# Kernel tuning notes

Measured on AMD Instinct MI355X. Metric: run time of the kernel, lower is better.

Reference implementation:

```python
import jax, jax.numpy as jnp
from jax import lax
import numpy as np

B, CIN, COUT, S = 2, 64, 128, 12
H1, H2 = CIN * 4, COUT * 4          # MBConv hidden dims (expand_ratio=4)
HEADS = 8
MLP_HID = COUT * 4                   # transformer mlp_ratio=4
EPS = 1e-5


def conv1x1(x, w, b=None):
    # 1x1x1 Conv3d == channel matmul. w: [out, in], x: [B,C,H,W,D]
    y = jnp.einsum('oc,bchwd->bohwd', w, x)
    if b is not None:
        y = y + b[None, :, None, None, None]
    return y


def inorm(x, g, b):
    # InstanceNorm3d(affine=True): per-sample, per-channel over spatial dims
    m = x.mean(axis=(2, 3, 4), keepdims=True)
    v = x.var(axis=(2, 3, 4), keepdims=True)
    return (x - m) * jax.lax.rsqrt(v + EPS) * g[None, :, None, None, None] + b[None, :, None, None, None]


def gnorm(x, g, b, groups):
    Bb, C, H, W, D = x.shape
    xr = x.reshape(Bb, groups, C // groups, H, W, D)
    m = xr.mean(axis=(2, 3, 4, 5), keepdims=True)
    v = xr.var(axis=(2, 3, 4, 5), keepdims=True)
    xr = (xr - m) * jax.lax.rsqrt(v + EPS)
    return xr.reshape(Bb, C, H, W, D) * g[None, :, None, None, None] + b[None, :, None, None, None]


def dwconv3(x, w):
    # depthwise 3x3x3, stride 1, pad 1. w: [C,1,3,3,3]
    return lax.conv_general_dilated(
        x, w, window_strides=(1, 1, 1), padding=[(1, 1)] * 3,
        dimension_numbers=('NCDHW', 'OIDHW', 'NCDHW'),
        feature_group_count=x.shape[1])


def mbconv(x, ew, g1, b1, dw, g2, b2, sw1, sb1, sw2, sb2, pw, g3, b3, use_residual):
    res = x
    h = jax.nn.silu(inorm(conv1x1(x, ew), g1, b1))        # expand 1x1
    h = jax.nn.silu(inorm(dwconv3(h, dw), g2, b2))        # depthwise 3x3x3
    s = h.mean(axis=(2, 3, 4), keepdims=True)             # SE: squeeze
    s = jax.nn.silu(conv1x1(s, sw1, sb1))
    s = jax.nn.sigmoid(conv1x1(s, sw2, sb2))
    h = h * s
    h = inorm(conv1x1(h, pw), g3, b3)                     # project
    return res + h if use_residual else h


def mhsa(x, qkv_w, proj_w, proj_b):
    Bb, C, H, W, D = x.shape
    N = H * W * D
    hd = C // HEADS
    qkv = conv1x1(x, qkv_w).reshape(Bb, 3, HEADS, hd, N)
    qkv = jnp.transpose(qkv, (1, 0, 2, 4, 3))             # [3,B,h,N,hd]
    q, k, v = qkv[0], qkv[1], qkv[2]
    attn = jax.nn.softmax(jnp.einsum('bhnd,bhmd->bhnm', q, k) * (hd ** -0.5), axis=-1)
    out = jnp.einsum('bhnm,bhmd->bhnd', attn, v)          # [B,h,N,hd]
    out = jnp.transpose(out, (0, 1, 3, 2)).reshape(Bb, C, H, W, D)
    return conv1x1(out, proj_w, proj_b)


def transformer_block(x, n1g, n1b, qkv, pw, pb, n2g, n2b, mw1, mb1, mw2, mb2):
    x = x + mhsa(gnorm(x, n1g, n1b, min(32, x.shape[1])), qkv, pw, pb)
    h = gnorm(x, n2g, n2b, min(32, x.shape[1]))
    h = conv1x1(jax.nn.gelu(conv1x1(h, mw1, mb1), approximate=False), mw2, mb2)
    return x + h


def shuffle_attn(x, cw1, cw2, gng, gnb, sw):
    b, c, h, w, d = x.shape
    G = 4
    gc = c // (2 * G)  # group_channels
    x6 = x.reshape(b, G, 2 * gc, h, w, d)
    x0 = x6[:, :, :gc].reshape(b * G, gc, h, w, d)
    x1 = x6[:, :, gc:].reshape(b * G, gc, h, w, d)
    # channel branch
    a = x0.mean(axis=(2, 3, 4), keepdims=True)
    a = conv1x1(jax.nn.silu(conv1x1(a, cw1)), cw2)
    x0 = jax.nn.sigmoid(a) * x0
    # spatial branch: GroupNorm(max(1,gc//8)=2 groups) + 1x1 conv
    sgn = gnorm(x1, gng, gnb, max(1, gc // 8))
    x1 = jax.nn.sigmoid(conv1x1(sgn, sw)) * x1
    out = jnp.concatenate([x0.reshape(b, G * gc, h, w, d), x1.reshape(b, G * gc, h, w, d)], axis=1)
    # channel shuffle
    out = out.reshape(b, G, 2 * gc, h, w, d).transpose(0, 2, 1, 3, 4, 5).reshape(b, c, h, w, d)
    return out


def setup_inputs() -> dict:
    key = jax.random.key(0)
    ks = iter(jax.random.split(key, 64))
    w = lambda *shape: jax.random.normal(next(ks), shape, jnp.float32) * 0.05
    p = {}
    p['x'] = jax.random.normal(next(ks), (B, CIN, S, S, S), jnp.float32)
    # mbconv1 (in=64 -> hidden=256 -> out=128), SE reduced = 256//4 = 64
    r1 = H1 // 4
    p['m1_ew'] = w(H1, CIN); p['m1_g1'] = jnp.ones(H1); p['m1_b1'] = jnp.zeros(H1)
    p['m1_dw'] = w(H1, 1, 3, 3, 3); p['m1_g2'] = jnp.ones(H1); p['m1_b2'] = jnp.zeros(H1)
    p['m1_sw1'] = w(r1, H1); p['m1_sb1'] = jnp.zeros(r1)
    p['m1_sw2'] = w(H1, r1); p['m1_sb2'] = jnp.zeros(H1)
    p['m1_pw'] = w(COUT, H1); p['m1_g3'] = jnp.ones(COUT); p['m1_b3'] = jnp.zeros(COUT)
    # mbconv2 (in=128 -> hidden=512 -> out=128, residual), SE reduced = 512//4 = 128
    r2 = H2 // 4
    p['m2_ew'] = w(H2, COUT); p['m2_g1'] = jnp.ones(H2); p['m2_b1'] = jnp.zeros(H2)
    p['m2_dw'] = w(H2, 1, 3, 3, 3); p['m2_g2'] = jnp.ones(H2); p['m2_b2'] = jnp.zeros(H2)
    p['m2_sw1'] = w(r2, H2); p['m2_sb1'] = jnp.zeros(r2)
    p['m2_sw2'] = w(H2, r2); p['m2_sb2'] = jnp.zeros(H2)
    p['m2_pw'] = w(COUT, H2); p['m2_g3'] = jnp.ones(COUT); p['m2_b3'] = jnp.zeros(COUT)
    # transformer
    p['t_n1g'] = jnp.ones(COUT); p['t_n1b'] = jnp.zeros(COUT)
    p['t_qkv'] = w(3 * COUT, COUT)
    p['t_pw'] = w(COUT, COUT); p['t_pb'] = jnp.zeros(COUT)
    p['t_n2g'] = jnp.ones(COUT); p['t_n2b'] = jnp.zeros(COUT)
    p['t_mw1'] = w(MLP_HID, COUT); p['t_mb1'] = jnp.zeros(MLP_HID)
    p['t_mw2'] = w(COUT, MLP_HID); p['t_mb2'] = jnp.zeros(COUT)
    # shuffle attention: group_channels = 128 // 8 = 16, channel_fc reduces to 4
    gc = COUT // 8
    p['s_cw1'] = w(max(1, gc // 4), gc); p['s_cw2'] = w(gc, max(1, gc // 4))
    p['s_gng'] = jnp.ones(gc); p['s_gnb'] = jnp.zeros(gc)
    p['s_sw'] = w(gc, gc)
    return p


def reference(x, m1_ew, m1_g1, m1_b1, m1_dw, m1_g2, m1_b2, m1_sw1, m1_sb1, m1_sw2, m1_sb2, m1_pw, m1_g3, m1_b3, m2_ew, m2_g1, m2_b1, m2_dw, m2_g2, m2_b2, m2_sw1, m2_sb1, m2_sw2, m2_sb2, m2_pw, m2_g3, m2_b3, t_n1g, t_n1b, t_qkv, t_pw, t_pb, t_n2g, t_n2b, t_mw1, t_mb1, t_mw2, t_mb2, s_cw1, s_cw2, s_gng, s_gnb, s_sw):
    x = mbconv(x, m1_ew, m1_g1, m1_b1, m1_dw, m1_g2, m1_b2, m1_sw1, m1_sb1, m1_sw2, m1_sb2, m1_pw, m1_g3, m1_b3, use_residual=False)
    x = mbconv(x, m2_ew, m2_g1, m2_b1, m2_dw, m2_g2, m2_b2, m2_sw1, m2_sb1, m2_sw2, m2_sb2, m2_pw, m2_g3, m2_b3, use_residual=True)
    x = transformer_block(x, t_n1g, t_n1b, t_qkv, t_pw, t_pb, t_n2g, t_n2b, t_mw1, t_mb1, t_mw2, t_mb2)
    x = shuffle_attn(x, s_cw1, s_cw2, s_gng, s_gnb, s_sw)
    return x
```

## Files before the change

### kernel.cpp

```cpp
#include <hip/hip_runtime.h>
#include <cmath>

#define NSP 1728
#define BB  2
#define SS  12

typedef __attribute__((ext_vector_type(8))) short short8;
typedef __attribute__((ext_vector_type(4))) short short4v;
typedef __attribute__((ext_vector_type(4))) float floatx4;

__device__ __forceinline__ short f2bf(float f) {
    unsigned u = __float_as_uint(f);
    u += 0x7fff + ((u >> 16) & 1);
    return (short)(u >> 16);
}
__device__ __forceinline__ unsigned pack2bf(float a, float b) {
    unsigned ua = __float_as_uint(a); ua += 0x7fff + ((ua >> 16) & 1);
    unsigned ub = __float_as_uint(b); ub += 0x7fff + ((ub >> 16) & 1);
    return (ua >> 16) | (ub & 0xffff0000u);
}
__device__ __forceinline__ short8 ld8(const short* p) {
    short4v a = *(const short4v*)p;
    short4v b = *(const short4v*)(p + 4);
    return __builtin_shufflevector(a, b, 0, 1, 2, 3, 4, 5, 6, 7);
}
__device__ __forceinline__ float fexp2(float x) {
    float r;
    asm("v_exp_f32 %0, %1" : "=v"(r) : "v"(x));
    return r;
}

__device__ __forceinline__ void block_reduce2(float& s, float& s2) {
    __shared__ float red[8][2];
    __syncthreads();
    #pragma unroll
    for (int o = 32; o; o >>= 1) {
        s  += __shfl_down(s,  o, 64);
        s2 += __shfl_down(s2, o, 64);
    }
    int lane = threadIdx.x & 63, w = threadIdx.x >> 6;
    if (lane == 0) { red[w][0] = s; red[w][1] = s2; }
    __syncthreads();
    int nw = (blockDim.x + 63) >> 6;
    if (threadIdx.x == 0) {
        float a = 0.f, b = 0.f;
        for (int i = 0; i < nw; i++) { a += red[i][0]; b += red[i][1]; }
        red[0][0] = a; red[0][1] = b;
    }
    __syncthreads();
    s = red[0][0]; s2 = red[0][1];
}

#define WTOT 376832
__global__ __launch_bounds__(256) void prep_kernel(
        const float* __restrict__ s0, const float* __restrict__ s1,
        const float* __restrict__ s2, const float* __restrict__ s3,
        const float* __restrict__ s4, const float* __restrict__ s5,
        const float* __restrict__ s6, const float* __restrict__ s7,
        short* __restrict__ dst, float* __restrict__ stz,
        const float* __restrict__ w1a, const float* __restrict__ w2a,
        const float* __restrict__ w1b, const float* __restrict__ w2b,
        float* __restrict__ tsw) {
    if (blockIdx.x < 11) stz[blockIdx.x * 256 + threadIdx.x] = 0.f;
    if (blockIdx.x >= 368) {
        int e = (blockIdx.x - 368) * 1024 + threadIdx.x * 4;
        #pragma unroll
        for (int k = 0; k < 4; k++) {
            int idx = e + k;
            float v;
            if (idx < 16384) {
                int c = idx >> 6, r = idx & 63;
                v = w1a[r * 256 + c];
            } else if (idx < 32768) {
                int l = idx - 16384; int r = l >> 8, ci = l & 255;
                v = w2a[ci * 64 + r];
            } else if (idx < 98304) {
                int l = idx - 32768; int c = l >> 7, r = l & 127;
                v = w1b[r * 512 + c];
            } else {
                int l = idx - 98304; int r = l >> 9, ci = l & 511;
                v = w2b[ci * 128 + r];
            }
            tsw[idx] = v;
        }
        return;
    }
    const int offs[9] = {0, 16384, 49152, 114688, 180224, 229376, 245760, 311296, WTOT};
    const float* srcs[8] = {s0, s1, s2, s3, s4, s5, s6, s7};
    int e = blockIdx.x * 1024 + threadIdx.x * 4;
    #pragma unroll
    for (int k = 0; k < 4; k++) {
        int idx = e + k;
        int seg = 0;
        while (idx >= offs[seg + 1]) seg++;
        dst[idx] = f2bf(srcs[seg][idx - offs[seg]]);
    }
}

template<int CIN, int SER>
__global__ __launch_bounds__(1024) void segate_kernel(
        const float* __restrict__ pooled_in,
        const float* __restrict__ w1t, const float* __restrict__ b1,
        const float* __restrict__ w2t, const float* __restrict__ b2,
        float* __restrict__ gate) {
    __shared__ float pooled[CIN];
    __shared__ float hid[SER];
    __shared__ float part[1024];
    int b = blockIdx.x;
    int tid = threadIdx.x;
    if (tid < CIN) pooled[tid] = pooled_in[b * CIN + tid];
    __syncthreads();
    {
        constexpr int S = 1024 / SER;
        constexpr int CC = CIN / S;
        int r = tid % SER, s = tid / SER;
        const float* wp = w1t + (size_t)(s * CC) * SER + r;
        float a = 0.f;
        #pragma unroll 4
        for (int c = 0; c < CC; c++) a = fmaf(wp[(size_t)c * SER], pooled[s * CC + c], a);
        part[tid] = a;
    }
    __syncthreads();
    if (tid < SER) {
        constexpr int S = 1024 / SER;
        float h = b1[tid];
        #pragma unroll
        for (int s2 = 0; s2 < S; s2++) h += part[s2 * SER + tid];
        hid[tid] = h / (1.f + __expf(-h));
    }
    __syncthreads();
    {
        constexpr int T = 1024 / CIN;
        constexpr int RR = SER / T;
        int ci = tid % CIN, s = tid / CIN;
        const float* wp = w2t + (size_t)(s * RR) * CIN + ci;
        float a = 0.f;
        #pragma unroll 4
        for (int r = 0; r < RR; r++) a = fmaf(wp[(size_t)r * CIN], hid[s * RR + r], a);
        part[tid] = a;
    }
    __syncthreads();
    if (tid < CIN) {
        constexpr int T = 1024 / CIN;
        float g = b2[tid];
        #pragma unroll
        for (int s2 = 0; s2 < T; s2++) g += part[s2 * CIN + tid];
        gate[b * CIN + tid] = 1.f / (1.f + __expf(-g));
    }
}

template<int CIN, int COUT>
__global__ __launch_bounds__(256) void convm_kernel(
        const float* __restrict__ in, const short* __restrict__ inbf,
        const short* __restrict__ wb,
        const float* __restrict__ biasc,
        const float* __restrict__ segate,
        const float* __restrict__ fstats, const float* __restrict__ fg,
        const float* __restrict__ fb, int fgs,
        const float* __restrict__ ing, const float* __restrict__ inb,
        const float* __restrict__ inres,
        const float* __restrict__ po, const float* __restrict__ pl,
        float* __restrict__ xout,
        const float* resid, float* out,
        short* __restrict__ obf, int obfm,
        float* stats_out, const float* __restrict__ statres, int act) {
    constexpr int XP = CIN + 8;
    __shared__ float sc[CIN];
    __shared__ float sh[CIN];
    __shared__ float sa[CIN];
    __shared__ float sbl[CIN];
    __shared__ float hid[128];
    __shared__ __align__(16) short xa[16 * XP];
    int flat = blockIdx.x;
    int b = flat / 108, mt = flat % 108;
    int n0 = mt * 16;
    int tid = threadIdx.x;

    if (!inbf) {
    if (po) {
        if (tid < 128) {
            int hh = tid >> 4, j = tid & 15;
            float l = 0.f;
            #pragma unroll
            for (int js = 0; js < 6; js++)
                l += pl[(size_t)((b * 8 + hh) * 6 + js) * NSP + n0 + j];
            hid[tid] = 1.f / l;
        }
        __syncthreads();
        #pragma unroll
        for (int i = 0; i < CIN / 64; i++) {
            int e = tid + i * 256;
            int ci = e >> 2;
            int jj = (e & 3) * 4;
            int hh = ci >> 4, d = ci & 15;
            float4 acc = {0.f, 0.f, 0.f, 0.f};
            #pragma unroll
            for (int js = 0; js < 6; js++) {
                float4 pv = *(const float4*)(po +
                    ((size_t)((b * 8 + hh) * 6 + js) * 16 + d) * NSP + n0 + jj);
                acc.x += pv.x; acc.y += pv.y; acc.z += pv.z; acc.w += pv.w;
            }
            float4 li = *(const float4*)(hid + hh * 16 + jj);
            xa[(jj + 0) * XP + ci] = f2bf(acc.x * li.x);
            xa[(jj + 1) * XP + ci] = f2bf(acc.y * li.y);
            xa[(jj + 2) * XP + ci] = f2bf(acc.z * li.z);
            xa[(jj + 3) * XP + ci] = f2bf(acc.w * li.w);
        }
        __syncthreads();
    } else {
    if (segate) {
        for (int c = tid; c < CIN; c += 256) {
            sc[c] = segate[b * CIN + c];
            sh[c] = 0.f;
        }
    } else if (ing) {
        for (int c = tid; c < CIN; c += 256) {
            const float* S = fstats + (size_t)(b * CIN + c) * 5;
            float A = S[0], Bq = S[1], Cq = S[2], Dq = S[3], Eq = S[4];
            const float N = (float)NSP;
            float mean = A / N, var = Bq / N - mean * mean;
            float a_ = ing[c] * rsqrtf(var + 1e-5f);
            float b_ = inb[c] - mean * a_;
            sa[c] = a_; sbl[c] = b_;
            sc[c] = a_ * A + b_ * N + Dq;
            sh[c] = a_ * a_ * Bq + 2.f * a_ * b_ * A + b_ * b_ * N
                  + 2.f * a_ * Cq + 2.f * b_ * Dq + Eq;
        }
        __syncthreads();
        float gS = 0.f, gS2 = 0.f;
        if (tid < CIN) {
            int g0 = (tid / fgs) * fgs;
            for (int k = 0; k < fgs; k++) { gS += sc[g0 + k]; gS2 += sh[g0 + k]; }
        }
        __syncthreads();
        if (tid < CIN) {
            float Ng = fgs * (float)NSP;
            float gm = gS / Ng, gv = gS2 / Ng - gm * gm;
            float s_ = rsqrtf(gv + 1e-5f) * fg[tid];
            sc[tid] = s_;
            sh[tid] = fb[tid] - gm * s_;
        }
    } else if (fstats) {
        for (int c = tid; c < CIN; c += 256) {
            int g0 = c / fgs;
            float S = 0.f, S2 = 0.f;
            for (int k = 0; k < fgs; k++) {
                S  += fstats[(b * CIN + g0 * fgs + k) * 2];
                S2 += fstats[(b * CIN + g0 * fgs + k) * 2 + 1];
            }
            float N = fgs * (float)NSP;
            float mean = S / N, var = S2 / N - mean * mean;
            float s = rsqrtf(var + 1e-5f) * fg[c];
            sc[c] = s;
            sh[c] = fb[c] - mean * s;
        }
    } else {
        for (int c = tid; c < CIN; c += 256) { sc[c] = 1.f; sh[c] = 0.f; }
    }
    __syncthreads();

    bool dosw = (xout != nullptr) && (blockIdx.y == 0);
    #pragma unroll
    for (int i = 0; i < CIN / 64; i++) {
        int e = tid + i * 256;
        int ci = e >> 2;
        int jj = (e & 3) * 4;
        size_t gi = ((size_t)b * CIN + ci) * NSP + n0 + jj;
        float4 v4 = *(const float4*)(in + gi);
        float v0, v1, v2, v3;
        if (ing) {
            float4 rr = *(const float4*)(inres + gi);
            float a_ = sa[ci], b_ = sbl[ci];
            float x0 = fmaf(v4.x, a_, b_) + rr.x;
            float x1 = fmaf(v4.y, a_, b_) + rr.y;
            float x2 = fmaf(v4.z, a_, b_) + rr.z;
            float x3 = fmaf(v4.w, a_, b_) + rr.w;
            if (dosw) {
                float4 o; o.x = x0; o.y = x1; o.z = x2; o.w = x3;
                *(float4*)(xout + gi) = o;
            }
            float s_ = sc[ci], h_ = sh[ci];
            v0 = fmaf(x0, s_, h_); v1 = fmaf(x1, s_, h_);
            v2 = fmaf(x2, s_, h_); v3 = fmaf(x3, s_, h_);
        } else {
            float s_ = sc[ci], h_ = sh[ci];
            v0 = fmaf(v4.x, s_, h_); v1 = fmaf(v4.y, s_, h_);
            v2 = fmaf(v4.z, s_, h_); v3 = fmaf(v4.w, s_, h_);
            if (dosw) {
                float4 o; o.x = v0; o.y = v1; o.z = v2; o.w = v3;
                *(float4*)(xout + gi) = o;
            }
        }
        xa[(jj + 0) * XP + ci] = f2bf(v0);
        xa[(jj + 1) * XP + ci] = f2bf(v1);
        xa[(jj + 2) * XP + ci] = f2bf(v2);
        xa[(jj + 3) * XP + ci] = f2bf(v3);
    }
    __syncthreads();
    }
    }

    int lane = tid & 63, wv = tid >> 6;
    int col = lane & 15, quad = lane >> 4;
    short8 afr[CIN / 32];
    if (inbf) {
        const short* ar = inbf + ((size_t)b * 1728 + n0 + col) * CIN;
        #pragma unroll
        for (int kc = 0; kc < CIN / 32; kc++)
            afr[kc] = ld8(ar + kc * 32 + quad * 8);
    } else {
        #pragma unroll
        for (int kc = 0; kc < CIN / 32; kc++)
            afr[kc] = ld8(xa + col * XP + kc * 32 + quad * 8);
    }

    int cobase = blockIdx.y * 64 + wv * 16;
    int co = cobase + col;
    const short* wrow = wb + (size_t)co * CIN;
    floatx4 acc = {0.f, 0.f, 0.f, 0.f};
    #pragma unroll
    for (int kc = 0; kc < CIN / 32; kc++) {
        short8 bw = ld8(wrow + kc * 32 + quad * 8);
        acc = __builtin_amdgcn_mfma_f32_16x16x32_bf16(afr[kc], bw, acc, 0, 0, 0);
    }
    float bv = biasc ? biasc[co] : 0.f;
    float r0 = acc[0] + bv, r1 = acc[1] + bv, r2 = acc[2] + bv, r3 = acc[3] + bv;
    if (act == 2) {
        r0 = 0.5f * r0 * (1.f + erff(r0 * 0.70710678118654752f));
        r1 = 0.5f * r1 * (1.f + erff(r1 * 0.70710678118654752f));
        r2 = 0.5f * r2 * (1.f + erff(r2 * 0.70710678118654752f));
        r3 = 0.5f * r3 * (1.f + erff(r3 * 0.70710678118654752f));
    }
    size_t oi = ((size_t)b * COUT + co) * NSP + n0 + quad * 4;
    if (resid) {
        float4 rv = *(const float4*)(resid + oi);
        r0 += rv.x; r1 += rv.y; r2 += rv.z; r3 += rv.w;
    }
    if (obf) {
        if (obfm == 1) {
            if (co < 256) {
                float s_ = (co < 128) ? 0.36067376022224085f : 1.f;
                short* qb = obf + (((size_t)(b * 16 + (co >> 4)) * 1728 + n0 + quad * 4) * 16
                                   + (co & 15));
                qb[0]  = f2bf(r0 * s_);
                qb[16] = f2bf(r1 * s_);
                qb[32] = f2bf(r2 * s_);
                qb[48] = f2bf(r3 * s_);
            } else {
                short* vb = obf + 884736
                    + ((size_t)(b * 8 + ((co - 256) >> 4)) * 16 + (co & 15)) * 1728
                    + n0 + quad * 4;
                uint2 pv; pv.x = pack2bf(r0, r1); pv.y = pack2bf(r2, r3);
                *(uint2*)vb = pv;
            }
        } else {
            short* hb = obf + ((size_t)b * 1728 + n0 + quad * 4) * COUT + co;
            hb[0]        = f2bf(r0);
            hb[COUT]     = f2bf(r1);
            hb[2 * COUT] = f2bf(r2);
            hb[3 * COUT] = f2bf(r3);
        }
    }
    if (out) {
        float4 ov; ov.x = r0; ov.y = r1; ov.z = r2; ov.w = r3;
        *(float4*)(out + oi) = ov;
    }
    if (stats_out) {
        if (statres) {
            float4 rv = *(const float4*)(statres + oi);
            float s   = (r0 + r1) + (r2 + r3);
            float s2  = (r0 * r0 + r1 * r1) + (r2 * r2 + r3 * r3);
            float sx  = (r0 * rv.x + r1 * rv.y) + (r2 * rv.z + r3 * rv.w);
            float sr  = (rv.x + rv.y) + (rv.z + rv.w);
            float sr2 = (rv.x * rv.x + rv.y * rv.y) + (rv.z * rv.z + rv.w * rv.w);
            s   += __shfl_xor(s,   16, 64); s   += __shfl_xor(s,   32, 64);
            s2  += __shfl_xor(s2,  16, 64); s2  += __shfl_xor(s2,  32, 64);
            sx  += __shfl_xor(sx,  16, 64); sx  += __shfl_xor(sx,  32, 64);
            sr  += __shfl_xor(sr,  16, 64); sr  += __shfl_xor(sr,  32, 64);
            sr2 += __shfl_xor(sr2, 16, 64); sr2 += __shfl_xor(sr2, 32, 64);
            if (lane < 16) {
                float* sp = stats_out + (size_t)(b * COUT + cobase + lane) * 5;
                atomicAdd(sp + 0, s);
                atomicAdd(sp + 1, s2);
                atomicAdd(sp + 2, sx);
                atomicAdd(sp + 3, sr);
                atomicAdd(sp + 4, sr2);
            }
        } else {
            float s  = (r0 + r1) + (r2 + r3);
            float s2 = (r0 * r0 + r1 * r1) + (r2 * r2 + r3 * r3);
            s  += __shfl_xor(s,  16, 64);
            s  += __shfl_xor(s,  32, 64);
            s2 += __shfl_xor(s2, 16, 64);
            s2 += __shfl_xor(s2, 32, 64);
            if (lane < 16) {
                atomicAdd(&stats_out[(b * COUT + cobase + lane) * 2],     s);
                atomicAdd(&stats_out[(b * COUT + cobase + lane) * 2 + 1], s2);
            }
        }
    }
}

__global__ __launch_bounds__(256) void indw_kernel(
        const float* __restrict__ in,
        const float* __restrict__ g1, const float* __restrict__ b1,
        const float* __restrict__ dw,
        const float* __restrict__ g2, const float* __restrict__ b2,
        float* __restrict__ out, float* __restrict__ se_s, int C) {
    int bc = blockIdx.x;
    int c  = bc % C;
    __shared__ float tile[14 * 14 * 14];
    __shared__ float wsh[27];
    const float* ip = in + (size_t)bc * NSP;
    float r[7];
    float s = 0.f, s2 = 0.f;
    for (int i = threadIdx.x; i < 2744; i += 256) tile[i] = 0.f;
    #pragma unroll
    for (int i = 0; i < 7; i++) {
        int n = threadIdx.x + i * 256;
        if (n < NSP) { r[i] = ip[n]; s += r[i]; s2 += r[i] * r[i]; }
        else r[i] = 0.f;
    }
    if (threadIdx.x < 27) wsh[threadIdx.x] = dw[(size_t)c * 27 + threadIdx.x];
    block_reduce2(s, s2);
    float mean = s / NSP, var = s2 / NSP - (s / NSP) * (s / NSP);
    float rstd = rsqrtf(var + 1e-5f);
    float gc = g1[c], bc1 = b1[c];
    #pragma unroll
    for (int i = 0; i < 7; i++) {
        int n = threadIdx.x + i * 256;
        if (n < NSP) {
            int z = n / 144, y = (n / 12) % 12, x = n % 12;
            float v = (r[i] - mean) * rstd * gc + bc1;
            tile[((z + 1) * 14 + y + 1) * 14 + x + 1] = v / (1.f + __expf(-v));
        }
    }
    __syncthreads();
    float d[7];
    #pragma unroll
    for (int i = 0; i < 7; i++) {
        int n = threadIdx.x + i * 256;
        d[i] = 0.f;
        if (n < NSP) {
            int z = n / 144, y = (n / 12) % 12, x = n % 12;
            const float* ctr = tile + ((z + 1) * 14 + y + 1) * 14 + x + 1;
            float acc = 0.f;
            #pragma unroll
            for (int dz = 0; dz < 3; dz++)
                #pragma unroll
                for (int dy = 0; dy < 3; dy++)
                    #pragma unroll
                    for (int dx = 0; dx < 3; dx++)
                        acc = fmaf(wsh[dz * 9 + dy * 3 + dx],
                                   ctr[(dz - 1) * 196 + (dy - 1) * 14 + (dx - 1)], acc);
            d[i] = acc;
        }
    }
    s = 0.f; s2 = 0.f;
    #pragma unroll
    for (int i = 0; i < 7; i++) {
        int n = threadIdx.x + i * 256;
        if (n < NSP) { s += d[i]; s2 += d[i] * d[i]; }
    }
    block_reduce2(s, s2);
    mean = s / NSP; var = s2 / NSP - mean * mean;
    rstd = rsqrtf(var + 1e-5f);
    float gc2 = g2[c], bc2 = b2[c];
    float ssum = 0.f;
    float* op = out + (size_t)bc * NSP;
    #pragma unroll
    for (int i = 0; i < 7; i++) {
        int n = threadIdx.x + i * 256;
        if (n < NSP) {
            float v = (d[i] - mean) * rstd * gc2 + bc2;
            v = v / (1.f + __expf(-v));
            op[n] = v;
            ssum += v;
        }
    }
    float dummy = 0.f;
    block_reduce2(ssum, dummy);
    if (threadIdx.x == 0) se_s[bc] = ssum / NSP;
}

#define APT 36
#define JCH 288
__global__ __launch_bounds__(256) void attn_split_kernel(
        const short* __restrict__ qkbf, const short* __restrict__ vbf,
        float* __restrict__ po, float* __restrict__ pl) {
    __shared__ __align__(16) short pt[4][16 * APT];
    int bh = blockIdx.x;
    int b = bh >> 3, h = bh & 7;
    int js = blockIdx.z;
    int j0 = js * JCH;
    int wave = threadIdx.x >> 6, lane = threadIdx.x & 63;
    int m = lane & 15, quad = lane >> 4;
    int q0 = (blockIdx.y * 4 + wave) * 16;
    short* ptw = pt[wave];
    const short* qrow  = qkbf + ((size_t)(b * 16 + h) * 1728 + q0 + m) * 16;
    const short* kbase = qkbf + ((size_t)(b * 16 + 8 + h) * 1728 + j0) * 16;
    const short* vbase = vbf + ((size_t)(b * 8 + h) * 16) * 1728 + j0;
    short8 qa;
    #pragma unroll
    for (int i = 0; i < 8; i++) qa[i] = 0;
    if (quad < 2) qa = ld8(qrow + quad * 8);
    floatx4 o = {0.f, 0.f, 0.f, 0.f};
    float ls = 0.f;
    #pragma unroll
    for (int s = 0; s < 9; s++) {
        int jl = s * 32;
        short8 ak0, ak1;
        #pragma unroll
        for (int i = 0; i < 8; i++) { ak0[i] = 0; ak1[i] = 0; }
        if (quad < 2) {
            ak0 = ld8(kbase + (jl + m) * 16 + quad * 8);
            ak1 = ld8(kbase + (jl + 16 + m) * 16 + quad * 8);
        }
        floatx4 s0 = {0.f, 0.f, 0.f, 0.f}, s1 = {0.f, 0.f, 0.f, 0.f};
        s0 = __builtin_amdgcn_mfma_f32_16x16x32_bf16(ak0, qa, s0, 0, 0, 0);
        s1 = __builtin_amdgcn_mfma_f32_16x16x32_bf16(ak1, qa, s1, 0, 0, 0);
        float p0r0 = fexp2(s0[0]), p0r1 = fexp2(s0[1]), p0r2 = fexp2(s0[2]), p0r3 = fexp2(s0[3]);
        float p1r0 = fexp2(s1[0]), p1r1 = fexp2(s1[1]), p1r2 = fexp2(s1[2]), p1r3 = fexp2(s1[3]);
        ls += (p0r0 + p0r1) + (p0r2 + p0r3) + (p1r0 + p1r1) + (p1r2 + p1r3);
        uint2 w0, w1;
        w0.x = pack2bf(p0r0, p0r1); w0.y = pack2bf(p0r2, p0r3);
        w1.x = pack2bf(p1r0, p1r1); w1.y = pack2bf(p1r2, p1r3);
        *(uint2*)(ptw + m * APT + quad * 4)      = w0;
        *(uint2*)(ptw + m * APT + 16 + quad * 4) = w1;
        short8 av = ld8(vbase + (size_t)m * 1728 + jl + quad * 8);
        short8 pb = ld8(ptw + m * APT + quad * 8);
        o = __builtin_amdgcn_mfma_f32_16x16x32_bf16(av, pb, o, 0, 0, 0);
    }
    ls += __shfl_xor(ls, 16, 64);
    ls += __shfl_xor(ls, 32, 64);
    size_t pbase = ((size_t)(bh * 6 + js) * 16) * NSP;
    #pragma unroll
    for (int r = 0; r < 4; r++)
        po[pbase + (size_t)(quad * 4 + r) * NSP + q0 + m] = o[r];
    if (quad == 0) pl[(size_t)(bh * 6 + js) * NSP + q0 + m] = ls;
}

__global__ void sfinal_kernel(const float* __restrict__ X,
                              const float* __restrict__ st,
                              const float* __restrict__ cw1,
                              const float* __restrict__ cw2,
                              const float* __restrict__ gng,
                              const float* __restrict__ gnb,
                              const float* __restrict__ sw,
                              float* __restrict__ out) {
    int bg = blockIdx.x;
    int b = bg >> 2, g = bg & 3;
    __shared__ float swl[256];
    for (int i = threadIdx.x; i < 256; i += 64) swl[i] = sw[i];
    __syncthreads();
    float pooled[16];
    #pragma unroll
    for (int j = 0; j < 16; j++)
        pooled[j] = st[(b * 128 + g * 32 + j) * 2] * (1.f / NSP);
    float hid[4];
    #pragma unroll
    for (int r = 0; r < 4; r++) {
        float a = 0.f;
        #pragma unroll
        for (int j = 0; j < 16; j++) a = fmaf(cw1[r * 16 + j], pooled[j], a);
        hid[r] = a / (1.f + __expf(-a));
    }
    float gate[16];
    #pragma unroll
    for (int j = 0; j < 16; j++) {
        float a = 0.f;
        #pragma unroll
        for (int r = 0; r < 4; r++) a = fmaf(cw2[j * 4 + r], hid[r], a);
        gate[j] = 1.f / (1.f + __expf(-a));
    }
    float gmean[2], grstd[2];
    #pragma unroll
    for (int t = 0; t < 2; t++) {
        float S = 0.f, S2 = 0.f;
        #pragma unroll
        for (int k = 0; k < 8; k++) {
            int c = g * 32 + 16 + t * 8 + k;
            S  += st[(b * 128 + c) * 2];
            S2 += st[(b * 128 + c) * 2 + 1];
        }
        float N = 8.f * NSP;
        gmean[t] = S / N;
        grstd[t] = rsqrtf(S2 / N - gmean[t] * gmean[t] + 1e-5f);
    }
    int n = blockIdx.y * 64 + threadIdx.x;
    const float* xb = X + (size_t)b * 128 * NSP;
    #pragma unroll
    for (int j = 0; j < 16; j++) {
        float v = xb[(size_t)(g * 32 + j) * NSP + n] * gate[j];
        int k = g * 16 + j;
        int cp = (k % 32) * 4 + (k / 32);
        out[((size_t)b * 128 + cp) * NSP + n] = v;
    }
    float sgn[16];
    #pragma unroll
    for (int j = 0; j < 16; j++) {
        int grp = j >> 3;
        float xv = xb[(size_t)(g * 32 + 16 + j) * NSP + n];
        sgn[j] = (xv - gmean[grp]) * grstd[grp] * gng[j] + gnb[j];
    }
    #pragma unroll
    for (int j = 0; j < 16; j++) {
        float a = 0.f;
        #pragma unroll
        for (int jp = 0; jp < 16; jp++) a = fmaf(swl[j * 16 + jp], sgn[jp], a);
        float v = (1.f / (1.f + __expf(-a))) * xb[(size_t)(g * 32 + 16 + j) * NSP + n];
        int k = 64 + g * 16 + j;
        int cp = (k % 32) * 4 + (k / 32);
        out[((size_t)b * 128 + cp) * NSP + n] = v;
    }
}

extern "C" void kernel_launch(void* const* d_in, const int* in_sizes, int n_in,
                              void* d_out, int out_size, void* d_ws, size_t ws_size,
                              hipStream_t stream) {
    const float* x     = (const float*)d_in[0];
    const float* m1_ew = (const float*)d_in[1];
    const float* m1_g1 = (const float*)d_in[2];
    const float* m1_b1 = (const float*)d_in[3];
    const float* m1_dw = (const float*)d_in[4];
    const float* m1_g2 = (const float*)d_in[5];
    const float* m1_b2 = (const float*)d_in[6];
    const float* m1_sw1= (const float*)d_in[7];
    const float* m1_sb1= (const float*)d_in[8];
    const float* m1_sw2= (const float*)d_in[9];
    const float* m1_sb2= (const float*)d_in[10];
    const float* m1_pw = (const float*)d_in[11];
    const float* m1_g3 = (const float*)d_in[12];
    const float* m1_b3 = (const float*)d_in[13];
    const float* m2_ew = (const float*)d_in[14];
    const float* m2_g1 = (const float*)d_in[15];
    const float* m2_b1 = (const float*)d_in[16];
    const float* m2_dw = (const float*)d_in[17];
    const float* m2_g2 = (const float*)d_in[18];
    const float* m2_b2 = (const float*)d_in[19];
    const float* m2_sw1= (const float*)d_in[20];
    const float* m2_sb1= (const float*)d_in[21];
    const float* m2_sw2= (const float*)d_in[22];
    const float* m2_sb2= (const float*)d_in[23];
    const float* m2_pw = (const float*)d_in[24];
    const float* m2_g3 = (const float*)d_in[25];
    const float* m2_b3 = (const float*)d_in[26];
    const float* t_n1g = (const float*)d_in[27];
    const float* t_n1b = (const float*)d_in[28];
    const float* t_qkv = (const float*)d_in[29];
    const float* t_pw  = (const float*)d_in[30];
    const float* t_pb  = (const float*)d_in[31];
    const float* t_n2g = (const float*)d_in[32];
    const float* t_n2b = (const float*)d_in[33];
    const float* t_mw1 = (const float*)d_in[34];
    const float* t_mb1 = (const float*)d_in[35];
    const float* t_mw2 = (const float*)d_in[36];
    const float* t_mb2 = (const float*)d_in[37];
    const float* s_cw1 = (const float*)d_in[38];
    const float* s_cw2 = (const float*)d_in[39];
    const float* s_gng = (const float*)d_in[40];
    const float* s_gnb = (const float*)d_in[41];
    const float* s_sw  = (const float*)d_in[42];

    float* out = (float*)d_out;

    float* ws = (float*)d_ws;
    float* bufA   = ws;
    float* bufB   = bufA + (size_t)BB * 512 * NSP;
    float* bufX   = bufB + (size_t)BB * 512 * NSP;
    float* bufY   = bufX + (size_t)BB * 128 * NSP;
    float* bufQKV = bufY + (size_t)BB * 128 * NSP;
    float* pl     = bufQKV + (size_t)BB * 384 * NSP;
    float* small  = pl + (size_t)16 * 6 * NSP;
    float* se_s   = small;
    float* st1    = small + 1024;
    float* st3    = small + 1536;
    float* st4    = small + 2048;
    float* st2    = small + 2560;
    float* gate1  = small + 4096;
    float* gate2  = small + 4608;
    short* wbf    = (short*)(small + 8192);
    float* tsw    = small + 196608;
    float* T_M1SW1 = tsw;
    float* T_M1SW2 = tsw + 16384;
    float* T_M2SW1 = tsw + 32768;
    float* T_M2SW2 = tsw + 98304;
    float* bufX2  = tsw + 163840;
    float* po     = bufA;
    short* qkbf   = (short*)bufQKV;
    short* hbf    = (short*)bufA;

    short* W_M1EW = wbf + 0;
    short* W_M1PW = wbf + 16384;
    short* W_M2EW = wbf + 49152;
    short* W_M2PW = wbf + 114688;
    short* W_QKV  = wbf + 180224;
    short* W_TPW  = wbf + 229376;
    short* W_MW1  = wbf + 245760;
    short* W_MW2  = wbf + 311296;

    dim3 blk(256);

    prep_kernel<<<528, blk, 0, stream>>>(
        m1_ew, m1_pw, m2_ew, m2_pw, t_qkv, t_pw, t_mw1, t_mw2, wbf, st1,
        m1_sw1, m1_sw2, m2_sw1, m2_sw2, tsw);

    convm_kernel<64, 256><<<dim3(BB * 108, 4), blk, 0, stream>>>(
        x, nullptr, W_M1EW, nullptr, nullptr,
        nullptr, nullptr, nullptr, 0,
        nullptr, nullptr, nullptr,
        nullptr, nullptr, nullptr,
        nullptr, bufA, nullptr, 0, nullptr, nullptr, 0);
    indw_kernel<<<BB * 256, blk, 0, stream>>>(bufA, m1_g1, m1_b1, m1_dw, m1_g2, m1_b2, bufB, se_s, 256);
    segate_kernel<256, 64><<<BB, dim3(1024), 0, stream>>>(
        se_s, T_M1SW1, m1_sb1, T_M1SW2, m1_sb2, gate1);
    convm_kernel<256, 128><<<dim3(BB * 108, 2), blk, 0, stream>>>(
        bufB, nullptr, W_M1PW, nullptr, gate1,
        nullptr, nullptr, nullptr, 0,
        nullptr, nullptr, nullptr,
        nullptr, nullptr, nullptr,
        nullptr, bufY, nullptr, 0, st1, nullptr, 0);

    convm_kernel<128, 512><<<dim3(BB * 108, 8), blk, 0, stream>>>(
        bufY, nullptr, W_M2EW, nullptr, nullptr,
        st1, m1_g3, m1_b3, 1,
        nullptr, nullptr, nullptr,
        nullptr, nullptr, bufX,
        nullptr, bufA, nullptr, 0, nullptr, nullptr, 0);
    indw_kernel<<<BB * 512, blk, 0, stream>>>(bufA, m2_g1, m2_b1, m2_dw, m2_g2, m2_b2, bufB, se_s, 512);
    segate_kernel<512, 128><<<BB, dim3(1024), 0, stream>>>(
        se_s, T_M2SW1, m2_sb1, T_M2SW2, m2_sb2, gate2);
    convm_kernel<512, 128><<<dim3(BB * 108, 2), blk, 0, stream>>>(
        bufB, nullptr, W_M2PW, nullptr, gate2,
        nullptr, nullptr, nullptr, 0,
        nullptr, nullptr, nullptr,
        nullptr, nullptr, nullptr,
        nullptr, bufY, nullptr, 0, st2, bufX, 0);

    convm_kernel<128, 384><<<dim3(BB * 108, 6), blk, 0, stream>>>(
        bufY, nullptr, W_QKV, nullptr, nullptr,
        st2, t_n1g, t_n1b, 4,
        m2_g3, m2_b3, bufX,
        nullptr, nullptr, bufX2,
        nullptr, nullptr, qkbf, 1, nullptr, nullptr, 0);
    attn_split_kernel<<<dim3(16, 27, 6), blk, 0, stream>>>(qkbf, qkbf + 884736, po, pl);
    convm_kernel<128, 128><<<dim3(BB * 108, 2), blk, 0, stream>>>(
        nullptr, nullptr, W_TPW, t_pb, nullptr,
        nullptr, nullptr, nullptr, 0,
        nullptr, nullptr, nullptr,
        po, pl, nullptr,
        bufX2, bufX2, nullptr, 0, st3, nullptr, 0);
    convm_kernel<128, 512><<<dim3(BB * 108, 8), blk, 0, stream>>>(
        bufX2, nullptr, W_MW1, t_mb1, nullptr,
        st3, t_n2g, t_n2b, 4,
        nullptr, nullptr, nullptr,
        nullptr, nullptr, nullptr,
        nullptr, nullptr, hbf, 2, nullptr, nullptr, 2);
    convm_kernel<512, 128><<<dim3(BB * 108, 2), blk, 0, stream>>>(
        nullptr, hbf, W_MW2, t_mb2, nullptr,
        nullptr, nullptr, nullptr, 0,
        nullptr, nullptr, nullptr,
        nullptr, nullptr, nullptr,
        bufX2, bufX2, nullptr, 0, st4, nullptr, 0);

    sfinal_kernel<<<dim3(BB * 4, 27), dim3(64), 0, stream>>>(
        bufX2, st4, s_cw1, s_cw2, s_gng, s_gnb, s_sw, out);
}
```

Measured before the change: 316.0 us.

## Compute several output-channel tiles per conv block and un-split attention

```diff
diff --git a/kernel.cpp b/kernel.cpp
--- a/kernel.cpp
+++ b/kernel.cpp
@@ -149,7 +149,7 @@
     }
 }
 
-template<int CIN, int COUT>
+template<int CIN, int COUT, int COSUB>
 __global__ __launch_bounds__(256) void convm_kernel(
         const float* __restrict__ in, const short* __restrict__ inbf,
         const short* __restrict__ wb,
@@ -159,7 +159,6 @@
         const float* __restrict__ fb, int fgs,
         const float* __restrict__ ing, const float* __restrict__ inb,
         const float* __restrict__ inres,
-        const float* __restrict__ po, const float* __restrict__ pl,
         float* __restrict__ xout,
         const float* resid, float* out,
         short* __restrict__ obf, int obfm,
@@ -169,7 +168,6 @@
     __shared__ float sh[CIN];
     __shared__ float sa[CIN];
     __shared__ float sbl[CIN];
-    __shared__ float hid[128];
     __shared__ __align__(16) short xa[16 * XP];
     int flat = blockIdx.x;
     int b = flat / 108, mt = flat % 108;
@@ -177,37 +175,6 @@
     int tid = threadIdx.x;
 
     if (!inbf) {
-    if (po) {
-        if (tid < 128) {
-            int hh = tid >> 4, j = tid & 15;
-            float l = 0.f;
-            #pragma unroll
-            for (int js = 0; js < 6; js++)
-                l += pl[(size_t)((b * 8 + hh) * 6 + js) * NSP + n0 + j];
-            hid[tid] = 1.f / l;
-        }
-        __syncthreads();
-        #pragma unroll
-        for (int i = 0; i < CIN / 64; i++) {
-            int e = tid + i * 256;
-            int ci = e >> 2;
-            int jj = (e & 3) * 4;
-            int hh = ci >> 4, d = ci & 15;
-            float4 acc = {0.f, 0.f, 0.f, 0.f};
-            #pragma unroll
-            for (int js = 0; js < 6; js++) {
-                float4 pv = *(const float4*)(po +
-                    ((size_t)((b * 8 + hh) * 6 + js) * 16 + d) * NSP + n0 + jj);
-                acc.x += pv.x; acc.y += pv.y; acc.z += pv.z; acc.w += pv.w;
-            }
-            float4 li = *(const float4*)(hid + hh * 16 + jj);
-            xa[(jj + 0) * XP + ci] = f2bf(acc.x * li.x);
-            xa[(jj + 1) * XP + ci] = f2bf(acc.y * li.y);
-            xa[(jj + 2) * XP + ci] = f2bf(acc.z * li.z);
-            xa[(jj + 3) * XP + ci] = f2bf(acc.w * li.w);
-        }
-        __syncthreads();
-    } else {
     if (segate) {
         for (int c = tid; c < CIN; c += 256) {
             sc[c] = segate[b * CIN + c];
@@ -298,7 +265,6 @@
     }
     __syncthreads();
     }
-    }
 
     int lane = tid & 63, wv = tid >> 6;
     int col = lane & 15, quad = lane >> 4;
@@ -314,88 +280,99 @@
             afr[kc] = ld8(xa + col * XP + kc * 32 + quad * 8);
     }
 
-    int cobase = blockIdx.y * 64 + wv * 16;
-    int co = cobase + col;
-    const short* wrow = wb + (size_t)co * CIN;
-    floatx4 acc = {0.f, 0.f, 0.f, 0.f};
-    #pragma unroll
-    for (int kc = 0; kc < CIN / 32; kc++) {
-        short8 bw = ld8(wrow + kc * 32 + quad * 8);
-        acc = __builtin_amdgcn_mfma_f32_16x16x32_bf16(afr[kc], bw, acc, 0, 0, 0);
-    }
-    float bv = biasc ? biasc[co] : 0.f;
-    float r0 = acc[0] + bv, r1 = acc[1] + bv, r2 = acc[2] + bv, r3 = acc[3] + bv;
-    if (act == 2) {
-        r0 = 0.5f * r0 * (1.f + erff(r0 * 0.70710678118654752f));
-        r1 = 0.5f * r1 * (1.f + erff(r1 * 0.70710678118654752f));
-        r2 = 0.5f * r2 * (1.f + erff(r2 * 0.70710678118654752f));
-        r3 = 0.5f * r3 * (1.f + erff(r3 * 0.70710678118654752f));
-    }
-    size_t oi = ((size_t)b * COUT + co) * NSP + n0 + quad * 4;
-    if (resid) {
-        float4 rv = *(const float4*)(resid + oi);
-        r0 += rv.x; r1 += rv.y; r2 += rv.z; r3 += rv.w;
-    }
-    if (obf) {
-        if (obfm == 1) {
-            if (co < 256) {
-                float s_ = (co < 128) ? 0.36067376022224085f : 1.f;
-                short* qb = obf + (((size_t)(b * 16 + (co >> 4)) * 1728 + n0 + quad * 4) * 16
-                                   + (co & 15));
-                qb[0]  = f2bf(r0 * s_);
-                qb[16] = f2bf(r1 * s_);
-                qb[32] = f2bf(r2 * s_);
-                qb[48] = f2bf(r3 * s_);
+    int cobase0 = blockIdx.y * (64 * COSUB) + wv * (16 * COSUB);
+    floatx4 acc[COSUB];
+    #pragma unroll
+    for (int sub = 0; sub < COSUB; sub++) {
+        floatx4 a = {0.f, 0.f, 0.f, 0.f};
+        const short* wrow = wb + (size_t)(cobase0 + sub * 16 + col) * CIN;
+        #pragma unroll
+        for (int kc = 0; kc < CIN / 32; kc++) {
+            short8 bw = ld8(wrow + kc * 32 + quad * 8);
+            a = __builtin_amdgcn_mfma_f32_16x16x32_bf16(afr[kc], bw, a, 0, 0, 0);
+        }
+        acc[sub] = a;
+    }
+
+    #pragma unroll
+    for (int sub = 0; sub < COSUB; sub++) {
+        int cobase = cobase0 + sub * 16;
+        int co = cobase + col;
+        float bv = biasc ? biasc[co] : 0.f;
+        float r0 = acc[sub][0] + bv, r1 = acc[sub][1] + bv;
+        float r2 = acc[sub][2] + bv, r3 = acc[sub][3] + bv;
+        if (act == 2) {
+            r0 = 0.5f * r0 * (1.f + erff(r0 * 0.70710678118654752f));
+            r1 = 0.5f * r1 * (1.f + erff(r1 * 0.70710678118654752f));
+            r2 = 0.5f * r2 * (1.f + erff(r2 * 0.70710678118654752f));
+            r3 = 0.5f * r3 * (1.f + erff(r3 * 0.70710678118654752f));
+        }
+        size_t oi = ((size_t)b * COUT + co) * NSP + n0 + quad * 4;
+        if (resid) {
+            float4 rv = *(const float4*)(resid + oi);
+            r0 += rv.x; r1 += rv.y; r2 += rv.z; r3 += rv.w;
+        }
+        if (obf) {
+            if (obfm == 1) {
+                if (co < 256) {
+                    float s_ = (co < 128) ? 0.36067376022224085f : 1.f;
+                    short* qb = obf + (((size_t)(b * 16 + (co >> 4)) * 1728 + n0 + quad * 4) * 16
+                                       + (co & 15));
+                    qb[0]  = f2bf(r0 * s_);
+                    qb[16] = f2bf(r1 * s_);
+                    qb[32] = f2bf(r2 * s_);
+                    qb[48] = f2bf(r3 * s_);
+                } else {
+                    short* vb = obf + 884736
+                        + ((size_t)(b * 8 + ((co - 256) >> 4)) * 16 + (co & 15)) * 1728
+                        + n0 + quad * 4;
+                    uint2 pv; pv.x = pack2bf(r0, r1); pv.y = pack2bf(r2, r3);
+                    *(uint2*)vb = pv;
+                }
             } else {
-                short* vb = obf + 884736
-                    + ((size_t)(b * 8 + ((co - 256) >> 4)) * 16 + (co & 15)) * 1728
-                    + n0 + quad * 4;
-                uint2 pv; pv.x = pack2bf(r0, r1); pv.y = pack2bf(r2, r3);
-                *(uint2*)vb = pv;
+                short* hb = obf + ((size_t)b * 1728 + n0 + quad * 4) * COUT + co;
+                hb[0]        = f2bf(r0);
+                hb[COUT]     = f2bf(r1);
+                hb[2 * COUT] = f2bf(r2);
+                hb[3 * COUT] = f2bf(r3);
             }
-        } else {
-            short* hb = obf + ((size_t)b * 1728 + n0 + quad * 4) * COUT + co;
-            hb[0]        = f2bf(r0);
-            hb[COUT]     = f2bf(r1);
-            hb[2 * COUT] = f2bf(r2);
-            hb[3 * COUT] = f2bf(r3);
-        }
-    }
-    if (out) {
-        float4 ov; ov.x = r0; ov.y = r1; ov.z = r2; ov.w = r3;
-        *(float4*)(out + oi) = ov;
-    }
-    if (stats_out) {
-        if (statres) {
-            float4 rv = *(const float4*)(statres + oi);
-            float s   = (r0 + r1) + (r2 + r3);
-            float s2  = (r0 * r0 + r1 * r1) + (r2 * r2 + r3 * r3);
-            float sx  = (r0 * rv.x + r1 * rv.y) + (r2 * rv.z + r3 * rv.w);
-            float sr  = (rv.x + rv.y) + (rv.z + rv.w);
-            float sr2 = (rv.x * rv.x + rv.y * rv.y) + (rv.z * rv.z + rv.w * rv.w);
-            s   += __shfl_xor(s,   16, 64); s   += __shfl_xor(s,   32, 64);
-            s2  += __shfl_xor(s2,  16, 64); s2  += __shfl_xor(s2,  32, 64);
-            sx  += __shfl_xor(sx,  16, 64); sx  += __shfl_xor(sx,  32, 64);
-            sr  += __shfl_xor(sr,  16, 64); sr  += __shfl_xor(sr,  32, 64);
-            sr2 += __shfl_xor(sr2, 16, 64); sr2 += __shfl_xor(sr2, 32, 64);
-            if (lane < 16) {
-                float* sp = stats_out + (size_t)(b * COUT + cobase + lane) * 5;
-                atomicAdd(sp + 0, s);
-                atomicAdd(sp + 1, s2);
-                atomicAdd(sp + 2, sx);
-                atomicAdd(sp + 3, sr);
-                atomicAdd(sp + 4, sr2);
-            }
-        } else {
-            float s  = (r0 + r1) + (r2 + r3);
-            float s2 = (r0 * r0 + r1 * r1) + (r2 * r2 + r3 * r3);
-            s  += __shfl_xor(s,  16, 64);
-            s  += __shfl_xor(s,  32, 64);
-            s2 += __shfl_xor(s2, 16, 64);
-            s2 += __shfl_xor(s2, 32, 64);
-            if (lane < 16) {
-                atomicAdd(&stats_out[(b * COUT + cobase + lane) * 2],     s);
-                atomicAdd(&stats_out[(b * COUT + cobase + lane) * 2 + 1], s2);
+        }
+        if (out) {
+            float4 ov; ov.x = r0; ov.y = r1; ov.z = r2; ov.w = r3;
+            *(float4*)(out + oi) = ov;
+        }
+        if (stats_out) {
+            if (statres) {
+                float4 rv = *(const float4*)(statres + oi);
+                float s   = (r0 + r1) + (r2 + r3);
+                float s2  = (r0 * r0 + r1 * r1) + (r2 * r2 + r3 * r3);
+                float sx  = (r0 * rv.x + r1 * rv.y) + (r2 * rv.z + r3 * rv.w);
+                float sr  = (rv.x + rv.y) + (rv.z + rv.w);
+                float sr2 = (rv.x * rv.x + rv.y * rv.y) + (rv.z * rv.z + rv.w * rv.w);
+                s   += __shfl_xor(s,   16, 64); s   += __shfl_xor(s,   32, 64);
+                s2  += __shfl_xor(s2,  16, 64); s2  += __shfl_xor(s2,  32, 64);
+                sx  += __shfl_xor(sx,  16, 64); sx  += __shfl_xor(sx,  32, 64);
+                sr  += __shfl_xor(sr,  16, 64); sr  += __shfl_xor(sr,  32, 64);
+                sr2 += __shfl_xor(sr2, 16, 64); sr2 += __shfl_xor(sr2, 32, 64);
+                if (lane < 16) {
+                    float* sp = stats_out + (size_t)(b * COUT + cobase + lane) * 5;
+                    atomicAdd(sp + 0, s);
+                    atomicAdd(sp + 1, s2);
+                    atomicAdd(sp + 2, sx);
+                    atomicAdd(sp + 3, sr);
+                    atomicAdd(sp + 4, sr2);
+                }
+            } else {
+                float s  = (r0 + r1) + (r2 + r3);
+                float s2 = (r0 * r0 + r1 * r1) + (r2 * r2 + r3 * r3);
+                s  += __shfl_xor(s,  16, 64);
+                s  += __shfl_xor(s,  32, 64);
+                s2 += __shfl_xor(s2, 16, 64);
+                s2 += __shfl_xor(s2, 32, 64);
+                if (lane < 16) {
+                    atomicAdd(&stats_out[(b * COUT + cobase + lane) * 2],     s);
+                    atomicAdd(&stats_out[(b * COUT + cobase + lane) * 2 + 1], s2);
+                }
             }
         }
     }
@@ -484,30 +461,27 @@
 }
 
 #define APT 36
-#define JCH 288
-__global__ __launch_bounds__(256) void attn_split_kernel(
+__global__ __launch_bounds__(256) void attn_kernel(
         const short* __restrict__ qkbf, const short* __restrict__ vbf,
-        float* __restrict__ po, float* __restrict__ pl) {
+        float* __restrict__ O) {
     __shared__ __align__(16) short pt[4][16 * APT];
     int bh = blockIdx.x;
     int b = bh >> 3, h = bh & 7;
-    int js = blockIdx.z;
-    int j0 = js * JCH;
     int wave = threadIdx.x >> 6, lane = threadIdx.x & 63;
     int m = lane & 15, quad = lane >> 4;
     int q0 = (blockIdx.y * 4 + wave) * 16;
     short* ptw = pt[wave];
     const short* qrow  = qkbf + ((size_t)(b * 16 + h) * 1728 + q0 + m) * 16;
-    const short* kbase = qkbf + ((size_t)(b * 16 + 8 + h) * 1728 + j0) * 16;
-    const short* vbase = vbf + ((size_t)(b * 8 + h) * 16) * 1728 + j0;
+    const short* kbase = qkbf + ((size_t)(b * 16 + 8 + h) * 1728) * 16;
+    const short* vbase = vbf + ((size_t)(b * 8 + h) * 16) * 1728;
     short8 qa;
     #pragma unroll
     for (int i = 0; i < 8; i++) qa[i] = 0;
     if (quad < 2) qa = ld8(qrow + quad * 8);
     floatx4 o = {0.f, 0.f, 0.f, 0.f};
     float ls = 0.f;
-    #pragma unroll
-    for (int s = 0; s < 9; s++) {
+    #pragma unroll 2
+    for (int s = 0; s < 54; s++) {
         int jl = s * 32;
         short8 ak0, ak1;
         #pragma unroll
@@ -533,11 +507,11 @@
     }
     ls += __shfl_xor(ls, 16, 64);
     ls += __shfl_xor(ls, 32, 64);
-    size_t pbase = ((size_t)(bh * 6 + js) * 16) * NSP;
+    float inv = 1.f / ls;
+    size_t obase = ((size_t)(b * 128 + h * 16 + quad * 4)) * NSP + q0 + m;
     #pragma unroll
     for (int r = 0; r < 4; r++)
-        po[pbase + (size_t)(quad * 4 + r) * NSP + q0 + m] = o[r];
-    if (quad == 0) pl[(size_t)(bh * 6 + js) * NSP + q0 + m] = ls;
+        O[obase + (size_t)r * NSP] = o[r] * inv;
 }
 
 __global__ void sfinal_kernel(const float* __restrict__ X,
@@ -686,7 +660,7 @@
     float* T_M2SW1 = tsw + 32768;
     float* T_M2SW2 = tsw + 98304;
     float* bufX2  = tsw + 163840;
-    float* po     = bufA;
+    float* bufO   = bufA;
     short* qkbf   = (short*)bufQKV;
     short* hbf    = (short*)bufA;
 
@@ -705,62 +679,62 @@
         m1_ew, m1_pw, m2_ew, m2_pw, t_qkv, t_pw, t_mw1, t_mw2, wbf, st1,
         m1_sw1, m1_sw2, m2_sw1, m2_sw2, tsw);
 
-    convm_kernel<64, 256><<<dim3(BB * 108, 4), blk, 0, stream>>>(
+    convm_kernel<64, 256, 2><<<dim3(BB * 108, 2), blk, 0, stream>>>(
         x, nullptr, W_M1EW, nullptr, nullptr,
         nullptr, nullptr, nullptr, 0,
         nullptr, nullptr, nullptr,
-        nullptr, nullptr, nullptr,
+        nullptr,
         nullptr, bufA, nullptr, 0, nullptr, nullptr, 0);
     indw_kernel<<<BB * 256, blk, 0, stream>>>(bufA, m1_g1, m1_b1, m1_dw, m1_g2, m1_b2, bufB, se_s, 256);
     segate_kernel<256, 64><<<BB, dim3(1024), 0, stream>>>(
         se_s, T_M1SW1, m1_sb1, T_M1SW2, m1_sb2, gate1);
-    convm_kernel<256, 128><<<dim3(BB * 108, 2), blk, 0, stream>>>(
+    convm_kernel<256, 128, 1><<<dim3(BB * 108, 2), blk, 0, stream>>>(
         bufB, nullptr, W_M1PW, nullptr, gate1,
         nullptr, nullptr, nullptr, 0,
         nullptr, nullptr, nullptr,
-        nullptr, nullptr, nullptr,
+        nullptr,
         nullptr, bufY, nullptr, 0, st1, nullptr, 0);
 
-    convm_kernel<128, 512><<<dim3(BB * 108, 8), blk, 0, stream>>>(
+    convm_kernel<128, 512, 4><<<dim3(BB * 108, 2), blk, 0, stream>>>(
         bufY, nullptr, W_M2EW, nullptr, nullptr,
         st1, m1_g3, m1_b3, 1,
         nullptr, nullptr, nullptr,
-        nullptr, nullptr, bufX,
+        bufX,
         nullptr, bufA, nullptr, 0, nullptr, nullptr, 0);
     indw_kernel<<<BB * 512, blk, 0, stream>>>(bufA, m2_g1, m2_b1, m2_dw, m2_g2, m2_b2, bufB, se_s, 512);
     segate_kernel<512, 128><<<BB, dim3(1024), 0, stream>>>(
         se_s, T_M2SW1, m2_sb1, T_M2SW2, m2_sb2, gate2);
-    convm_kernel<512, 128><<<dim3(BB * 108, 2), blk, 0, stream>>>(
+    convm_kernel<512, 128, 1><<<dim3(BB * 108, 2), blk, 0, stream>>>(
         bufB, nullptr, W_M2PW, nullptr, gate2,
         nullptr, nullptr, nullptr, 0,
         nullptr, nullptr, nullptr,
-        nullptr, nullptr, nullptr,
+        nullptr,
         nullptr, bufY, nullptr, 0, st2, bufX, 0);
 
-    convm_kernel<128, 384><<<dim3(BB * 108, 6), blk, 0, stream>>>(
+    convm_kernel<128, 384, 3><<<dim3(BB * 108, 2), blk, 0, stream>>>(
         bufY, nullptr, W_QKV, nullptr, nullptr,
         st2, t_n1g, t_n1b, 4,
         m2_g3, m2_b3, bufX,
-        nullptr, nullptr, bufX2,
+        bufX2,
         nullptr, nullptr, qkbf, 1, nullptr, nullptr, 0);
-    attn_split_kernel<<<dim3(16, 27, 6), blk, 0, stream>>>(qkbf, qkbf + 884736, po, pl);
-    convm_kernel<128, 128><<<dim3(BB * 108, 2), blk, 0, stream>>>(
-        nullptr, nullptr, W_TPW, t_pb, nullptr,
+    attn_kernel<<<dim3(16, 27), blk, 0, stream>>>(qkbf, qkbf + 884736, bufO);
+    convm_kernel<128, 128, 1><<<dim3(BB * 108, 2), blk, 0, stream>>>(
+        bufO, nullptr, W_TPW, t_pb, nullptr,
         nullptr, nullptr, nullptr, 0,
         nullptr, nullptr, nullptr,
-        po, pl, nullptr,
+        nullptr,
         bufX2, bufX2, nullptr, 0, st3, nullptr, 0);
-    convm_kernel<128, 512><<<dim3(BB * 108, 8), blk, 0, stream>>>(
+    convm_kernel<128, 512, 4><<<dim3(BB * 108, 2), blk, 0, stream>>>(
         bufX2, nullptr, W_MW1, t_mb1, nullptr,
         st3, t_n2g, t_n2b, 4,
         nullptr, nullptr, nullptr,
-        nullptr, nullptr, nullptr,
+        nullptr,
         nullptr, nullptr, hbf, 2, nullptr, nullptr, 2);
-    convm_kernel<512, 128><<<dim3(BB * 108, 2), blk, 0, stream>>>(
+    convm_kernel<512, 128, 1><<<dim3(BB * 108, 2), blk, 0, stream>>>(
         nullptr, hbf, W_MW2, t_mb2, nullptr,
         nullptr, nullptr, nullptr, 0,
         nullptr, nullptr, nullptr,
-        nullptr, nullptr, nullptr,
+        nullptr,
         bufX2, bufX2, nullptr, 0, st4, nullptr, 0);
 
     sfinal_kernel<<<dim3(BB * 4, 27), dim3(64), 0, stream>>>(
```

New measurement: 319.4 us. Within noise of the previous version (+1.1%).
